# Performance work log

Measured on AMD Instinct MI355X. Metric: run time of the kernel, lower is better.

## Reference

```python
import jax, jax.numpy as jnp
import numpy as np

V, D, J = 1024, 1024, 1024  # num_outputs, predictor_dim, joiner_dim
B, U = 64, 512
NULL_INDEX = 0


def setup_inputs() -> dict:
    key = jax.random.key(0)
    ks = jax.random.split(key, 9)
    s = 0.02
    return {
        "y": jax.random.randint(ks[0], (B, U), 0, V, dtype=jnp.int64) if jax.config.jax_enable_x64 else jax.random.randint(ks[0], (B, U), 0, V, dtype=jnp.int32),
        "embed": jax.random.normal(ks[1], (V, D), jnp.float32) * s,
        "weight_ih": jax.random.normal(ks[2], (3 * D, D), jnp.float32) * s,
        "bias_ih": jax.random.normal(ks[3], (3 * D,), jnp.float32) * s,
        "weight_hh": jax.random.normal(ks[4], (3 * D, D), jnp.float32) * s,
        "bias_hh": jax.random.normal(ks[5], (3 * D,), jnp.float32) * s,
        "linear_w": jax.random.normal(ks[6], (J, D), jnp.float32) * s,
        "linear_b": jax.random.normal(ks[7], (J,), jnp.float32) * s,
        "initial_state": jax.random.normal(ks[8], (D,), jnp.float32),
    }


def reference(y, embed, weight_ih, bias_ih, weight_hh, bias_hh, linear_w, linear_b, initial_state):
    b, u_len = y.shape
    d = initial_state.shape[0]
    # Decoder input sequence: start symbol (NULL_INDEX=0) then the labels -> length U+1
    tokens = jnp.concatenate([jnp.full((b, 1), NULL_INDEX, dtype=y.dtype), y], axis=1)  # [B, U+1]
    x = embed[tokens]  # [B, U+1, D]
    # Precompute input-side gate pre-activations for all steps (batched GEMM)
    gx = jnp.einsum("bud,gd->bug", x, weight_ih) + bias_ih  # [B, U+1, 3D]
    h0 = jnp.broadcast_to(initial_state, (b, d))

    def step(h, gx_t):
        # PyTorch GRUCell: gates ordered (r, z, n)
        gh = h @ weight_hh.T + bias_hh  # [B, 3D]
        r = jax.nn.sigmoid(gx_t[:, :d] + gh[:, :d])
        z = jax.nn.sigmoid(gx_t[:, d:2 * d] + gh[:, d:2 * d])
        n = jnp.tanh(gx_t[:, 2 * d:] + r * gh[:, 2 * d:])
        h_new = (1.0 - z) * n + z * h
        return h_new, h_new

    _, hs = jax.lax.scan(step, h0, jnp.swapaxes(gx, 0, 1))  # hs: [U+1, B, D]
    out = jnp.einsum("ubd,jd->buj", hs, linear_w) + linear_b  # [B, U+1, J]
    return out
```

## Files before the change

### kernel.cpp

```cpp
#include <hip/hip_runtime.h>
#include <hip/hip_bf16.h>

typedef float f32x4 __attribute__((ext_vector_type(4)));
typedef short s16x8 __attribute__((ext_vector_type(8)));
typedef int   i32x4 __attribute__((ext_vector_type(4)));
typedef _Float16 h16x8 __attribute__((ext_vector_type(8)));

#define NV 1024
#define ND 1024
#define NJ 1024
#define NB 64
#define NU 512
#define NT 513
#define G3 3072
#define SLOT 65536
#define NWG 64

static __device__ __forceinline__ unsigned short f2h(float f) {
  union { _Float16 h; unsigned short u; } x; x.h = (_Float16)f;
  return x.u;
}

static __device__ __forceinline__ void unswizzle(long e, int& r, int& k) {
  long blk = e >> 9; int l = (int)((e >> 3) & 63); int j = (int)(e & 7);
  r = (int)(blk >> 5) * 16 + (l & 15);
  k = ((int)(blk & 31)) * 32 + ((l >> 4) << 3) + j;
}

__global__ void predictor_prep(const float* __restrict__ whh, const float* __restrict__ wih,
                               const float* __restrict__ em, const float* __restrict__ lw,
                               const float* __restrict__ bih, const float* __restrict__ bhh,
                               const float* __restrict__ init,
                               unsigned short* __restrict__ wh_sw, unsigned short* __restrict__ wi_sw,
                               unsigned short* __restrict__ em_sw, unsigned short* __restrict__ lw_sw,
                               float* __restrict__ bias_sum, unsigned short* __restrict__ hs,
                               unsigned int* __restrict__ flags) {
  long e = (long)blockIdx.x * 256 + threadIdx.x;
  const long nbig = 3145728, nsm = 1048576;
  if (e < nbig) { int r, k; unswizzle(e, r, k); wh_sw[e] = f2h(whh[(long)r * 1024 + k]); return; }
  e -= nbig;
  if (e < nbig) { int r, k; unswizzle(e, r, k); wi_sw[e] = f2h(wih[(long)r * 1024 + k]); return; }
  e -= nbig;
  if (e < nsm) { int r, k; unswizzle(e, r, k); em_sw[e] = f2h(em[(long)r * 1024 + k]); return; }
  e -= nsm;
  if (e < nsm) { int r, k; unswizzle(e, r, k); lw_sw[e] = f2h(lw[(long)r * 1024 + k]); return; }
  e -= nsm;
  if (e < 65536) { int r, k; unswizzle(e, r, k); hs[e] = f2h(init[k]); return; }
  e -= 65536;
  if (e < 3072) { bias_sum[e] = bih[e] + bhh[e]; return; }
  e -= 3072;
  if (e < 128) flags[e] = 0u;
}

__global__ __launch_bounds__(256) void predictor_gemm(
    const unsigned short* __restrict__ A, long a_chunk_stride,
    const unsigned short* __restrict__ Bw,
    const float* __restrict__ bias, float* __restrict__ out,
    int rowmul_i, int rowmul_c, int out_stride) {
  const int nt = blockIdx.x, chunk = blockIdx.y;
  const int tid = threadIdx.x, lane = tid & 63, wave = tid >> 6;
  const unsigned short* Ab = A + (long)chunk * a_chunk_stride + wave * 16384 + lane * 8;
  const unsigned short* Bb = Bw + (long)nt * 65536 + lane * 8;
  f32x4 a0 = {0,0,0,0}, a1 = {0,0,0,0}, a2 = {0,0,0,0}, a3 = {0,0,0,0};
#pragma unroll 4
  for (int kc = 0; kc < 32; ++kc) {
    h16x8 av = __builtin_bit_cast(h16x8, *(const s16x8*)(Ab + kc * 512));
    h16x8 w0 = __builtin_bit_cast(h16x8, *(const s16x8*)(Bb + kc * 512));
    h16x8 w1 = __builtin_bit_cast(h16x8, *(const s16x8*)(Bb + 16384 + kc * 512));
    h16x8 w2 = __builtin_bit_cast(h16x8, *(const s16x8*)(Bb + 32768 + kc * 512));
    h16x8 w3 = __builtin_bit_cast(h16x8, *(const s16x8*)(Bb + 49152 + kc * 512));
    a0 = __builtin_amdgcn_mfma_f32_16x16x32_f16(av, w0, a0, 0, 0, 0);
    a1 = __builtin_amdgcn_mfma_f32_16x16x32_f16(av, w1, a1, 0, 0, 0);
    a2 = __builtin_amdgcn_mfma_f32_16x16x32_f16(av, w2, a2, 0, 0, 0);
    a3 = __builtin_amdgcn_mfma_f32_16x16x32_f16(av, w3, a3, 0, 0, 0);
  }
  const int q = lane >> 4, nl = lane & 15, colbase = nt << 6;
#pragma unroll
  for (int j = 0; j < 4; ++j) {
    int il = (wave << 4) + (q << 2) + j;
    long row = (long)il * rowmul_i + (long)chunk * rowmul_c;
    float* orow = out + row * out_stride + colbase;
    orow[nl]      = a0[j] + bias[colbase + nl];
    orow[16 + nl] = a1[j] + bias[colbase + 16 + nl];
    orow[32 + nl] = a2[j] + bias[colbase + 32 + nl];
    orow[48 + nl] = a3[j] + bias[colbase + 48 + nl];
  }
}

#define PINSTAGE(CNT, B)                                                        \
  asm volatile("s_waitcnt vmcnt(" #CNT ")"                                      \
    : "+v"(hf[(B)*8+0]), "+v"(hf[(B)*8+1]), "+v"(hf[(B)*8+2]), "+v"(hf[(B)*8+3]), \
      "+v"(hf[(B)*8+4]), "+v"(hf[(B)*8+5]), "+v"(hf[(B)*8+6]), "+v"(hf[(B)*8+7]) :: "memory")

__global__ __launch_bounds__(256, 1) void predictor_rnn(
    const unsigned short* __restrict__ wh_sw, const float* __restrict__ gtab,
    const int* __restrict__ y, const float* __restrict__ init,
    unsigned short* __restrict__ hs, unsigned short* __restrict__ flags) {
  __shared__ unsigned short wlds[49152];
  __shared__ unsigned short tbuf[1024];
  const int wg = blockIdx.x, tid = threadIdx.x, lane = tid & 63, w = tid >> 6;
  const int q = lane >> 4, dloc = lane & 15, dg = (wg << 4) + dloc;

  for (int g = 0; g < 3; ++g) {
    const unsigned short* src = wh_sw + ((long)(g * 64 + wg) << 14);
#pragma unroll
    for (int i = 0; i < 8; ++i) {
      int c = i * 256 + tid;
      *(s16x8*)&wlds[g * 16384 + c * 8] = *(const s16x8*)&src[c * 8];
    }
  }
  __syncthreads();

  float hreg[4];
#pragma unroll
  for (int j = 0; j < 4; ++j) hreg[j] = init[dg];

  const unsigned short* fpoll = flags + (w << 6) + lane;
  unsigned short* fpub = flags + (w << 6) + wg;
  const s16x8* wbase = (const s16x8*)wlds + lane;

  for (int t = 1; t <= NT; ++t) {
    float gr[4], gz[4], gn[4];
#pragma unroll
    for (int j = 0; j < 4; ++j) {
      int b = (w << 4) + (q << 2) + j;
      int tok = (t == 1) ? 0 : y[b * NU + (t - 2)];
      const float* g = gtab + (long)tok * G3 + dg;
      asm volatile("global_load_dword %0, %1, off" : "=v"(gr[j]) : "v"(g) : "memory");
      asm volatile("global_load_dword %0, %1, off" : "=v"(gz[j]) : "v"(g + 1024) : "memory");
      asm volatile("global_load_dword %0, %1, off" : "=v"(gn[j]) : "v"(g + 2048) : "memory");
    }

    if (t > 1) {
      const unsigned int tm1 = (unsigned)(t - 1);
      for (;;) {
        unsigned int v;
        asm volatile("global_load_ushort %0, %1, off sc1" : "=v"(v) : "v"(fpoll) : "memory");
        asm volatile("s_waitcnt vmcnt(0)" : "+v"(v) :: "memory");
        if (__all((int)(v >= tm1))) break;
        __builtin_amdgcn_s_sleep(1);
      }
    }
    asm volatile("s_waitcnt vmcnt(0)"
      : "+v"(gr[0]), "+v"(gr[1]), "+v"(gr[2]), "+v"(gr[3]),
        "+v"(gz[0]), "+v"(gz[1]), "+v"(gz[2]), "+v"(gz[3]),
        "+v"(gn[0]), "+v"(gn[1]), "+v"(gn[2]), "+v"(gn[3]) :: "memory");

    const unsigned short* hprev = hs + (long)(t - 1) * SLOT + (w << 14);
    unsigned short* hcur = hs + (long)t * SLOT;

    i32x4 hf[32];
#pragma unroll
    for (int i = 0; i < 32; ++i) {
      const unsigned short* a = hprev + i * 512 + lane * 8;
      asm volatile("global_load_dwordx4 %0, %1, off sc1" : "=v"(hf[i]) : "v"(a) : "memory");
    }
    f32x4 aR = {0,0,0,0}, aZ = {0,0,0,0}, aN = {0,0,0,0};
    {
      PINSTAGE(24, 0);
#pragma unroll
      for (int i = 0; i < 8; ++i) { int kc = i; h16x8 a = __builtin_bit_cast(h16x8, hf[kc]);
        h16x8 wr = __builtin_bit_cast(h16x8, wbase[kc * 64]);
        h16x8 wz = __builtin_bit_cast(h16x8, wbase[2048 + kc * 64]);
        h16x8 wn = __builtin_bit_cast(h16x8, wbase[4096 + kc * 64]);
        aR = __builtin_amdgcn_mfma_f32_16x16x32_f16(a, wr, aR, 0, 0, 0);
        aZ = __builtin_amdgcn_mfma_f32_16x16x32_f16(a, wz, aZ, 0, 0, 0);
        aN = __builtin_amdgcn_mfma_f32_16x16x32_f16(a, wn, aN, 0, 0, 0); }
      PINSTAGE(16, 1);
#pragma unroll
      for (int i = 0; i < 8; ++i) { int kc = 8 + i; h16x8 a = __builtin_bit_cast(h16x8, hf[kc]);
        h16x8 wr = __builtin_bit_cast(h16x8, wbase[kc * 64]);
        h16x8 wz = __builtin_bit_cast(h16x8, wbase[2048 + kc * 64]);
        h16x8 wn = __builtin_bit_cast(h16x8, wbase[4096 + kc * 64]);
        aR = __builtin_amdgcn_mfma_f32_16x16x32_f16(a, wr, aR, 0, 0, 0);
        aZ = __builtin_amdgcn_mfma_f32_16x16x32_f16(a, wz, aZ, 0, 0, 0);
        aN = __builtin_amdgcn_mfma_f32_16x16x32_f16(a, wn, aN, 0, 0, 0); }
      PINSTAGE(8, 2);
#pragma unroll
      for (int i = 0; i < 8; ++i) { int kc = 16 + i; h16x8 a = __builtin_bit_cast(h16x8, hf[kc]);
        h16x8 wr = __builtin_bit_cast(h16x8, wbase[kc * 64]);
        h16x8 wz = __builtin_bit_cast(h16x8, wbase[2048 + kc * 64]);
        h16x8 wn = __builtin_bit_cast(h16x8, wbase[4096 + kc * 64]);
        aR = __builtin_amdgcn_mfma_f32_16x16x32_f16(a, wr, aR, 0, 0, 0);
        aZ = __builtin_amdgcn_mfma_f32_16x16x32_f16(a, wz, aZ, 0, 0, 0);
        aN = __builtin_amdgcn_mfma_f32_16x16x32_f16(a, wn, aN, 0, 0, 0); }
      PINSTAGE(0, 3);
#pragma unroll
      for (int i = 0; i < 8; ++i) { int kc = 24 + i; h16x8 a = __builtin_bit_cast(h16x8, hf[kc]);
        h16x8 wr = __builtin_bit_cast(h16x8, wbase[kc * 64]);
        h16x8 wz = __builtin_bit_cast(h16x8, wbase[2048 + kc * 64]);
        h16x8 wn = __builtin_bit_cast(h16x8, wbase[4096 + kc * 64]);
        aR = __builtin_amdgcn_mfma_f32_16x16x32_f16(a, wr, aR, 0, 0, 0);
        aZ = __builtin_amdgcn_mfma_f32_16x16x32_f16(a, wz, aZ, 0, 0, 0);
        aN = __builtin_amdgcn_mfma_f32_16x16x32_f16(a, wn, aN, 0, 0, 0); }
    }

#pragma unroll
    for (int j = 0; j < 4; ++j) {
      float r = 1.f / (1.f + __expf(-(gr[j] + aR[j])));
      float z = 1.f / (1.f + __expf(-(gz[j] + aZ[j])));
      float np = gn[j] + r * aN[j];
      float e2 = __expf(-2.f * fabsf(np));
      float tn = (1.f - e2) / (1.f + e2);
      tn = np < 0.f ? -tn : tn;
      float hnew = (1.f - z) * tn + z * hreg[j];
      hreg[j] = hnew;
      tbuf[(w << 8) + ((((q << 2) + j) | ((dloc >> 3) << 4)) << 3) + (dloc & 7)] = f2h(hnew);
    }
    asm volatile("s_waitcnt lgkmcnt(0)" ::: "memory");

    {
      unsigned long long pv = *(const unsigned long long*)(tbuf + (w << 8) + lane * 4);
      unsigned short* gp = hcur + ((long)(w * 32 + (wg >> 1)) << 9) + ((wg & 1) << 8) + lane * 4;
      asm volatile("global_store_dwordx2 %0, %1, off sc1" :: "v"(gp), "v"(pv) : "memory");
      asm volatile("s_waitcnt vmcnt(0)" ::: "memory");
      if (lane == 0)
        asm volatile("global_store_short %0, %1, off sc1" :: "v"(fpub), "v"((unsigned)t) : "memory");
    }
  }
}

extern "C" void kernel_launch(void* const* d_in, const int* in_sizes, int n_in,
                              void* d_out, int out_size, void* d_ws, size_t ws_size,
                              hipStream_t stream) {
  const int*   y    = (const int*)d_in[0];
  const float* em   = (const float*)d_in[1];
  const float* wih  = (const float*)d_in[2];
  const float* bih  = (const float*)d_in[3];
  const float* whh  = (const float*)d_in[4];
  const float* bhh  = (const float*)d_in[5];
  const float* lw   = (const float*)d_in[6];
  const float* lb   = (const float*)d_in[7];
  const float* init = (const float*)d_in[8];
  float* out = (float*)d_out;

  char* ws = (char*)d_ws;
  size_t off = 0;
  auto alloc = [&](size_t n) { void* p = ws + off; off += (n + 255) & ~(size_t)255; return p; };
  unsigned short* wh_sw   = (unsigned short*)alloc(6291456);
  unsigned short* wi_sw   = (unsigned short*)alloc(6291456);
  unsigned short* em_sw   = (unsigned short*)alloc(2097152);
  unsigned short* lw_sw   = (unsigned short*)alloc(2097152);
  float*          gtab    = (float*)alloc(12582912);
  float*          bias_sum= (float*)alloc(12288);
  unsigned int*   flags   = (unsigned int*)alloc(512);
  unsigned short* hs      = (unsigned short*)alloc(67371008UL);
  (void)ws_size; (void)in_sizes; (void)n_in; (void)out_size;

  predictor_prep<<<dim3(33037), dim3(256), 0, stream>>>(
      whh, wih, em, lw, bih, bhh, init, wh_sw, wi_sw, em_sw, lw_sw, bias_sum, hs, flags);
  predictor_gemm<<<dim3(48, 16), dim3(256), 0, stream>>>(
      em_sw, 65536L, wi_sw, bias_sum, gtab, 1, 64, 3072);
  predictor_rnn<<<dim3(NWG), dim3(256), 0, stream>>>(
      wh_sw, gtab, y, init, hs, (unsigned short*)flags);
  predictor_gemm<<<dim3(16, 513), dim3(256), 0, stream>>>(
      hs + 65536, 65536L, lw_sw, lb, out, 513, 1, 1024);
}
```

Before: 2.876 ms.

## Replace per-step flag handshake with canary-filled hidden-state polling

Drops the separate flag array and its publish store, which needed a vmcnt(0) wait before each flag write. Instead, every hidden-state slot is pre-filled with a canary pattern (0x7FFF halves, which is NaN in fp16), and consumers poll the previous step's data directly until no canary words remain. This removes one global round-trip from each recurrent step's critical path. In exchange, the prep kernel must write about 67 MB of canary data. Correctness also relies on real fp16 values never matching the canary and on each dword store becoming visible atomically.

```diff
diff --git a/kernel.cpp b/kernel.cpp
--- a/kernel.cpp
+++ b/kernel.cpp
@@ -15,6 +15,7 @@
 #define G3 3072
 #define SLOT 65536
 #define NWG 64
+#define CANARY 0x7FFF7FFFu
 
 static __device__ __forceinline__ unsigned short f2h(float f) {
   union { _Float16 h; unsigned short u; } x; x.h = (_Float16)f;
@@ -33,8 +34,7 @@
                                const float* __restrict__ init,
                                unsigned short* __restrict__ wh_sw, unsigned short* __restrict__ wi_sw,
                                unsigned short* __restrict__ em_sw, unsigned short* __restrict__ lw_sw,
-                               float* __restrict__ bias_sum, unsigned short* __restrict__ hs,
-                               unsigned int* __restrict__ flags) {
+                               float* __restrict__ bias_sum, unsigned short* __restrict__ hs) {
   long e = (long)blockIdx.x * 256 + threadIdx.x;
   const long nbig = 3145728, nsm = 1048576;
   if (e < nbig) { int r, k; unswizzle(e, r, k); wh_sw[e] = f2h(whh[(long)r * 1024 + k]); return; }
@@ -49,7 +49,11 @@
   e -= 65536;
   if (e < 3072) { bias_sum[e] = bih[e] + bhh[e]; return; }
   e -= 3072;
-  if (e < 128) flags[e] = 0u;
+  if (e < 4202496) {
+    s16x8 c = { (short)0x7FFF, (short)0x7FFF, (short)0x7FFF, (short)0x7FFF,
+                (short)0x7FFF, (short)0x7FFF, (short)0x7FFF, (short)0x7FFF };
+    *(s16x8*)(hs + 65536 + e * 8) = c;
+  }
 }
 
 __global__ __launch_bounds__(256) void predictor_gemm(
@@ -95,7 +99,7 @@
 __global__ __launch_bounds__(256, 1) void predictor_rnn(
     const unsigned short* __restrict__ wh_sw, const float* __restrict__ gtab,
     const int* __restrict__ y, const float* __restrict__ init,
-    unsigned short* __restrict__ hs, unsigned short* __restrict__ flags) {
+    unsigned short* __restrict__ hs) {
   __shared__ unsigned short wlds[49152];
   __shared__ unsigned short tbuf[1024];
   const int wg = blockIdx.x, tid = threadIdx.x, lane = tid & 63, w = tid >> 6;
@@ -115,8 +119,6 @@
 #pragma unroll
   for (int j = 0; j < 4; ++j) hreg[j] = init[dg];
 
-  const unsigned short* fpoll = flags + (w << 6) + lane;
-  unsigned short* fpub = flags + (w << 6) + wg;
   const s16x8* wbase = (const s16x8*)wlds + lane;
 
   for (int t = 1; t <= NT; ++t) {
@@ -131,23 +133,33 @@
       asm volatile("global_load_dword %0, %1, off" : "=v"(gn[j]) : "v"(g + 2048) : "memory");
     }
 
+    const unsigned short* hprev = hs + (long)(t - 1) * SLOT + (w << 14);
+    unsigned short* hcur = hs + (long)t * SLOT;
+
     if (t > 1) {
-      const unsigned int tm1 = (unsigned)(t - 1);
+      const unsigned int* sp = (const unsigned int*)hprev + (lane << 7);
       for (;;) {
-        unsigned int v;
-        asm volatile("global_load_ushort %0, %1, off sc1" : "=v"(v) : "v"(fpoll) : "memory");
-        asm volatile("s_waitcnt vmcnt(0)" : "+v"(v) :: "memory");
-        if (__all((int)(v >= tm1))) break;
-        __builtin_amdgcn_s_sleep(1);
+        unsigned int s0, s1, s2, s3, s4, s5, s6, s7;
+        asm volatile("global_load_dword %0, %1, off sc1" : "=v"(s0) : "v"(sp +   0) : "memory");
+        asm volatile("global_load_dword %0, %1, off sc1" : "=v"(s1) : "v"(sp +  16) : "memory");
+        asm volatile("global_load_dword %0, %1, off sc1" : "=v"(s2) : "v"(sp +  32) : "memory");
+        asm volatile("global_load_dword %0, %1, off sc1" : "=v"(s3) : "v"(sp +  48) : "memory");
+        asm volatile("global_load_dword %0, %1, off sc1" : "=v"(s4) : "v"(sp +  64) : "memory");
+        asm volatile("global_load_dword %0, %1, off sc1" : "=v"(s5) : "v"(sp +  80) : "memory");
+        asm volatile("global_load_dword %0, %1, off sc1" : "=v"(s6) : "v"(sp +  96) : "memory");
+        asm volatile("global_load_dword %0, %1, off sc1" : "=v"(s7) : "v"(sp + 112) : "memory");
+        asm volatile("s_waitcnt vmcnt(0)"
+          : "+v"(s0), "+v"(s1), "+v"(s2), "+v"(s3),
+            "+v"(s4), "+v"(s5), "+v"(s6), "+v"(s7) :: "memory");
+        int ok = (s0 != CANARY) & (s1 != CANARY) & (s2 != CANARY) & (s3 != CANARY) &
+                 (s4 != CANARY) & (s5 != CANARY) & (s6 != CANARY) & (s7 != CANARY);
+        if (__all(ok)) break;
       }
     }
     asm volatile("s_waitcnt vmcnt(0)"
       : "+v"(gr[0]), "+v"(gr[1]), "+v"(gr[2]), "+v"(gr[3]),
         "+v"(gz[0]), "+v"(gz[1]), "+v"(gz[2]), "+v"(gz[3]),
         "+v"(gn[0]), "+v"(gn[1]), "+v"(gn[2]), "+v"(gn[3]) :: "memory");
-
-    const unsigned short* hprev = hs + (long)(t - 1) * SLOT + (w << 14);
-    unsigned short* hcur = hs + (long)t * SLOT;
 
     i32x4 hf[32];
 #pragma unroll
@@ -213,9 +225,6 @@
       unsigned long long pv = *(const unsigned long long*)(tbuf + (w << 8) + lane * 4);
       unsigned short* gp = hcur + ((long)(w * 32 + (wg >> 1)) << 9) + ((wg & 1) << 8) + lane * 4;
       asm volatile("global_store_dwordx2 %0, %1, off sc1" :: "v"(gp), "v"(pv) : "memory");
-      asm volatile("s_waitcnt vmcnt(0)" ::: "memory");
-      if (lane == 0)
-        asm volatile("global_store_short %0, %1, off sc1" :: "v"(fpub), "v"((unsigned)t) : "memory");
     }
   }
 }
@@ -243,16 +252,14 @@
   unsigned short* lw_sw   = (unsigned short*)alloc(2097152);
   float*          gtab    = (float*)alloc(12582912);
   float*          bias_sum= (float*)alloc(12288);
-  unsigned int*   flags   = (unsigned int*)alloc(512);
   unsigned short* hs      = (unsigned short*)alloc(67371008UL);
   (void)ws_size; (void)in_sizes; (void)n_in; (void)out_size;
 
-  predictor_prep<<<dim3(33037), dim3(256), 0, stream>>>(
-      whh, wih, em, lw, bih, bhh, init, wh_sw, wi_sw, em_sw, lw_sw, bias_sum, hs, flags);
+  predictor_prep<<<dim3(49452), dim3(256), 0, stream>>>(
+      whh, wih, em, lw, bih, bhh, init, wh_sw, wi_sw, em_sw, lw_sw, bias_sum, hs);
   predictor_gemm<<<dim3(48, 16), dim3(256), 0, stream>>>(
       em_sw, 65536L, wi_sw, bias_sum, gtab, 1, 64, 3072);
-  predictor_rnn<<<dim3(NWG), dim3(256), 0, stream>>>(
-      wh_sw, gtab, y, init, hs, (unsigned short*)flags);
+  predictor_rnn<<<dim3(NWG), dim3(256), 0, stream>>>(wh_sw, gtab, y, init, hs);
   predictor_gemm<<<dim3(16, 513), dim3(256), 0, stream>>>(
       hs + 65536, 65536L, lw_sw, lb, out, 513, 1, 1024);
 }
```

Measured after the change: 3.038 ms. 1.06x slower.
